# Kernel optimization log

Measured on AMD Instinct MI355X. Metric: run time of the kernel, lower is better.

## Reference

```python
import jax, jax.numpy as jnp
import numpy as np

B, S, NGB, NG, DIM = 64, 4096, 13, 48, 3
NCH = [8, 8, 1]
NSHELLS = 8


def setup_inputs() -> dict:
    key = jax.random.key(0)
    ks = jax.random.split(key, 16)
    rng = np.random.default_rng(0)
    # valid row-wise permutations of the N_ngb neighbor slots per group op
    GnnPerms = jnp.asarray(np.argsort(rng.random((NG, NGB)), axis=1), dtype=jnp.int64)
    NNSites = jax.random.randint(ks[0], (NGB, S), 0, S, dtype=jnp.int64)
    SitesToShells = jax.random.randint(ks[1], (S,), 0, NSHELLS, dtype=jnp.int64)
    # block-diagonal (Ng*dim, Ng*dim) cartesian rotation blocks
    blk = rng.normal(size=(NG, DIM, DIM)).astype(np.float32) * 0.5
    gd = np.zeros((NG * DIM, NG * DIM), np.float32)
    for g in range(NG):
        gd[g * DIM:(g + 1) * DIM, g * DIM:(g + 1) * DIM] = blk[g]
    gdiags = jnp.asarray(gd)
    std = 0.2
    return {
        "InStates": jax.random.normal(ks[2], (B, 1, S), jnp.float32),
        "Psi0": jax.random.normal(ks[3], (NCH[0], 1, NGB), jnp.float32) * std,
        "bias0": jax.random.normal(ks[4], (NCH[0], 1), jnp.float32) * std,
        "Psi1": jax.random.normal(ks[5], (NCH[1], NCH[0], NGB), jnp.float32) * std,
        "bias1": jax.random.normal(ks[6], (NCH[1], 1), jnp.float32) * std,
        "Psi2": jax.random.normal(ks[7], (NCH[2], NCH[1], NGB), jnp.float32) * std,
        "bias2": jax.random.normal(ks[8], (NCH[2], 1), jnp.float32) * std,
        "wtVC": jax.random.normal(ks[9], (DIM, NGB), jnp.float32) * std,
        "ShellWeights": jax.random.normal(ks[10], (NSHELLS,), jnp.float32) * std,
        "gdiags": gdiags,
        "GnnPerms": GnnPerms,
        "NNSites": NNSites,
        "SitesToShells": SitesToShells,
    }


def _rearrange(x, NNSites):
    # x: (B, Nch, S) -> (B, Nch*N_ngb, S); subchannel j of channel c holds x[b, c, NNSites[j, s]]
    b, c, s = x.shape
    return x[:, :, NNSites].reshape(b, c * NGB, s)


def _gconv(x, W, b):
    # x: (B, NchIn*N_ngb, S); W: (NchOut, NchIn, N_ngb); b: (NchOut, 1)
    # group-rotated weights: GW[o, g, c*N_ngb+j] = W[o, c, GnnPerms[g, j]]
    GW = _gconv.GW_cache  # set per-call below via closure-free pattern; replaced in reference
    raise NotImplementedError


def reference(InStates, Psi0, bias0, Psi1, bias1, Psi2, bias2, wtVC,
              ShellWeights, gdiags, GnnPerms, NNSites, SitesToShells):
    act = jax.nn.softplus

    def gconv(x, W, b):
        # rotated weights: (NchOut, Ng, NchIn*N_ngb)
        GW = W[:, :, GnnPerms].transpose(0, 2, 1, 3).reshape(W.shape[0], NG, -1)
        h = jnp.einsum('ogk,bks->bogs', GW, x) + b[:, :, None]  # (B, NchOut, Ng, S)
        return act(h).mean(axis=2)                               # group-orbit average

    out = _rearrange(InStates, NNSites)
    for W, b in ((Psi0, bias0), (Psi1, bias1), (Psi2, bias2)):
        out = gconv(out, W, b)                 # (B, NchOut, S)
        out = _rearrange(out, NNSites)         # (B, NchOut*N_ngb, S)
    # vector channel: row g*dim+d of P is wtVC[d, GnnPerms[g]]
    P = wtVC[:, GnnPerms].transpose(1, 0, 2).reshape(NG * DIM, NGB)
    Wvc = gdiags @ P                           # (Ng*dim, N_ngb)
    v = jnp.einsum('kn,bns->bks', Wvc, out)    # (B, Ng*dim, S)
    v = v.reshape(-1, NG, DIM, out.shape[-1]).mean(axis=1)  # (B, dim, S)
    v = v * ShellWeights[SitesToShells]        # per-site shell weighting
    return v.sum(axis=2) / out.shape[-1]       # (B, dim)
```

## Files before the change

kernel.cpp:

```cpp
#include <hip/hip_runtime.h>
#include <hip/hip_bf16.h>

#define BATCH 64
#define SITES 4096
#define NGB 13
#define NGRP 48
#define SDIM 3

typedef __bf16 bf16x8 __attribute__((ext_vector_type(8)));
typedef float  f32x4  __attribute__((ext_vector_type(4)));

#define OFF_AVC  0
#define OFF_U    64
#define OFF_A0   67648
#define OFF_A1   2164800
#define OFF_PART 4261952
#define UW0H 0
#define UW0L 12288
#define UW1H 24576
#define UW1L 73728
#define UW2H 122880
#define UW2L 129024

__device__ __forceinline__ float softplus_f(float h) {
    return fmaxf(h, 0.f) + __logf(1.f + __expf(-fabsf(h)));
}

__global__ __launch_bounds__(256) void precompute_kernel(
    const float* __restrict__ Psi0, const float* __restrict__ Psi1,
    const float* __restrict__ Psi2, const float* __restrict__ wtVC,
    const float* __restrict__ gdiags, const int* __restrict__ perms,
    float* __restrict__ ws)
{
    float*  Avc = ws + OFF_AVC;
    __bf16* U   = (__bf16*)(ws + OFF_U);
    int t = blockIdx.x * 256 + threadIdx.x;
    if (t < 12288) {
        int k = t & 31, row = t >> 5;
        int o = row / NGRP, g = row - o * NGRP;
        float w = (k < NGB) ? Psi0[o * NGB + perms[g * NGB + k]] : 0.f;
        __bf16 hi = (__bf16)w;
        U[UW0H + t] = hi;
        U[UW0L + t] = (__bf16)(w - (float)hi);
    } else if (t < 61440) {
        int u = t - 12288;
        int k = u & 127, row = u >> 7;
        int o = row / NGRP, g = row - o * NGRP;
        float w = 0.f;
        if (k < 104) { int j = k >> 3, c = k & 7;
                       w = Psi1[(o * 8 + c) * NGB + perms[g * NGB + j]]; }
        __bf16 hi = (__bf16)w;
        U[UW1H + u] = hi;
        U[UW1L + u] = (__bf16)(w - (float)hi);
    } else if (t < 67584) {
        int u = t - 61440;
        int k = u & 127, g = u >> 7;
        float w = 0.f;
        if (k < 104) { int j = k >> 3, c = k & 7;
                       w = Psi2[c * NGB + perms[g * NGB + j]]; }
        __bf16 hi = (__bf16)w;
        U[UW2H + u] = hi;
        U[UW2L + u] = (__bf16)(w - (float)hi);
    } else if (t < 67584 + 39 * NGRP) {
        int t2 = t - 67584;
        int g = t2 % NGRP, u = t2 / NGRP;
        int d = u / NGB, n = u % NGB;
        const int row = g * SDIM + d;
        float s = 0.f;
        for (int k = 0; k < NGRP * SDIM; k++) {
            int g2 = k / SDIM, d2 = k - g2 * SDIM;
            float p = wtVC[d2 * NGB + perms[g2 * NGB + n]];
            s = fmaf(gdiags[row * (NGRP * SDIM) + k], p, s);
        }
        atomicAdd(&Avc[u], s * (1.f / 48.f));
    }
}

template<int NCIN, int NCTOT, int CT, int KPAD, int KSTR, int NWAVES, int NWN,
         int CHUNKS>
__global__ __launch_bounds__(NWAVES * 64) void layer_mfma(
    const float* __restrict__ prev,
    const __bf16* __restrict__ Wh,
    const __bf16* __restrict__ Wl,
    const float* __restrict__ bias,
    const int*   __restrict__ NN,
    float* __restrict__ out)
{
    constexpr int NTHR   = NWAVES * 64;
    constexpr int M      = NCTOT * NGRP;
    constexpr int MTILES = M / 16, NTILES = CT / 16;
    constexpr int NWM    = NWAVES / NWN;
    constexpr int MT_W   = MTILES / NWM, NT_W = NTILES / NWN;
    constexpr int KT     = KPAD / 32;
    constexpr int GS     = NGB * CT;
    constexpr int SPT    = (GS + NTHR - 1) / NTHR;
    constexpr int CPB    = SITES / CT;
    constexpr int BUF    = CT * KSTR;
    constexpr int BPB    = CPB / CHUNKS;

    static_assert(MT_W * 16 == NGRP, "wave covers exactly one o");
    static_assert(NWM * MT_W == MTILES && NWN * NT_W == NTILES, "");
    static_assert((KPAD & 31) == 0 && (KSTR & 7) == 0, "");
    static_assert(CPB % CHUNKS == 0, "block stays within one batch");

    __shared__ __bf16 xh_lds[2 * BUF];
    __shared__ __bf16 xl_lds[2 * BUF];

    const int tid  = threadIdx.x;
    const int wave = tid >> 6, lane = tid & 63;
    const int m16  = lane & 15, quad = lane >> 4;

    const int bid    = blockIdx.x;
    const int b      = bid / BPB;
    const int octet  = bid % BPB;
    const int s0base = octet * (CHUNKS * CT);

    int sj[SPT], scol[SPT];
    bool sv[SPT];
#pragma unroll
    for (int i = 0; i < SPT; i++) {
        int site = tid + i * NTHR;
        sv[i] = (site < GS);
        int ss = sv[i] ? site : 0;
        sj[i] = ss / CT;
        scol[i] = ss % CT;
    }

    auto stage_site = [&](int i, int nn, __bf16* dh, __bf16* dl) {
        if constexpr (NCIN == 1) {
            float v = prev[(size_t)b * SITES + nn];
            __bf16 hi = (__bf16)v;
            dh[scol[i] * KSTR + sj[i]] = hi;
            dl[scol[i] * KSTR + sj[i]] = (__bf16)(v - (float)hi);
        } else {
            const float4* p4 = (const float4*)(prev + ((size_t)(b * SITES + nn)) * 8);
            float4 u0 = p4[0], u1 = p4[1];
            float v[8] = {u0.x, u0.y, u0.z, u0.w, u1.x, u1.y, u1.z, u1.w};
            bf16x8 hv, lv;
#pragma unroll
            for (int c8 = 0; c8 < 8; c8++) {
                __bf16 hi = (__bf16)v[c8];
                hv[c8] = hi;
                lv[c8] = (__bf16)(v[c8] - (float)hi);
            }
            *(bf16x8*)(dh + scol[i] * KSTR + sj[i] * 8) = hv;
            *(bf16x8*)(dl + scol[i] * KSTR + sj[i] * 8) = lv;
        }
    };

    if constexpr (NCIN == 1) {
        for (int e = tid; e < 2 * CT * (KPAD - NGB); e += NTHR) {
            int buf = e / (CT * (KPAD - NGB));
            int r   = e % (CT * (KPAD - NGB));
            int col = r / (KPAD - NGB), p = r % (KPAD - NGB);
            xh_lds[buf * BUF + col * KSTR + NGB + p] = (__bf16)0.f;
            xl_lds[buf * BUF + col * KSTR + NGB + p] = (__bf16)0.f;
        }
    } else {
        const bf16x8 z8 = {};
        for (int e = tid; e < 2 * CT * 3; e += NTHR) {
            int buf = e / (CT * 3);
            int r   = e % (CT * 3);
            int col = r % CT, z = r / CT;
            *(bf16x8*)(xh_lds + buf * BUF + col * KSTR + 104 + z * 8) = z8;
            *(bf16x8*)(xl_lds + buf * BUF + col * KSTR + 104 + z * 8) = z8;
        }
    }

#pragma unroll
    for (int i = 0; i < SPT; i++) if (sv[i]) {
        int nn = NN[sj[i] * SITES + s0base + scol[i]];
        stage_site(i, nn, xh_lds, xl_lds);
    }
    int nnA[SPT];
    if (CHUNKS > 1) {
        const int s1 = s0base + CT;
#pragma unroll
        for (int i = 0; i < SPT; i++)
            nnA[i] = sv[i] ? NN[sj[i] * SITES + s1 + scol[i]] : 0;
    }
    __syncthreads();

    const int wave_mt0 = (wave / NWN) * MT_W;
    const int wave_nt0 = (wave % NWN) * NT_W;
    const int o_g      = (wave_mt0 * 16) / NGRP;
    const float bo     = bias[o_g];

#pragma unroll 1
    for (int c = 0; c < CHUNKS; c++) {
        const int cur = c & 1;
        const __bf16* xh = xh_lds + cur * BUF;
        const __bf16* xl = xl_lds + cur * BUF;

        f32x4 acc[MT_W][NT_W];
#pragma unroll
        for (int mt = 0; mt < MT_W; mt++)
#pragma unroll
            for (int nt = 0; nt < NT_W; nt++) acc[mt][nt] = (f32x4){0.f, 0.f, 0.f, 0.f};

#pragma unroll
        for (int kt = 0; kt < KT; kt++) {
            const int koff = kt * 32 + quad * 8;
            bf16x8 ah[MT_W], al[MT_W], bh[NT_W], bl[NT_W];
#pragma unroll
            for (int mt = 0; mt < MT_W; mt++) {
                int row = (wave_mt0 + mt) * 16 + m16;
                ah[mt] = *(const bf16x8*)(Wh + (size_t)row * KPAD + koff);
                al[mt] = *(const bf16x8*)(Wl + (size_t)row * KPAD + koff);
            }
#pragma unroll
            for (int nt = 0; nt < NT_W; nt++) {
                int cbase = ((wave_nt0 + nt) * 16 + m16) * KSTR + koff;
                bh[nt] = *(const bf16x8*)(xh + cbase);
                bl[nt] = *(const bf16x8*)(xl + cbase);
            }
#pragma unroll
            for (int mt = 0; mt < MT_W; mt++)
#pragma unroll
                for (int nt = 0; nt < NT_W; nt++)
                    acc[mt][nt] = __builtin_amdgcn_mfma_f32_16x16x32_bf16(
                        ah[mt], bh[nt], acc[mt][nt], 0, 0, 0);
#pragma unroll
            for (int mt = 0; mt < MT_W; mt++)
#pragma unroll
                for (int nt = 0; nt < NT_W; nt++)
                    acc[mt][nt] = __builtin_amdgcn_mfma_f32_16x16x32_bf16(
                        al[mt], bh[nt], acc[mt][nt], 0, 0, 0);
#pragma unroll
            for (int mt = 0; mt < MT_W; mt++)
#pragma unroll
                for (int nt = 0; nt < NT_W; nt++)
                    acc[mt][nt] = __builtin_amdgcn_mfma_f32_16x16x32_bf16(
                        ah[mt], bl[nt], acc[mt][nt], 0, 0, 0);
        }

        const int s0c = s0base + c * CT;
#pragma unroll
        for (int nt = 0; nt < NT_W; nt++) {
            float s = 0.f;
#pragma unroll
            for (int mt = 0; mt < MT_W; mt++)
#pragma unroll
                for (int r = 0; r < 4; r++)
                    s += softplus_f(acc[mt][nt][r] + bo);
            s += __shfl_xor(s, 16);
            s += __shfl_xor(s, 32);
            if (quad == 0)
                out[((size_t)(b * SITES + s0c + (wave_nt0 + nt) * 16 + m16)) * NCTOT + o_g]
                    = s * (1.f / 48.f);
        }

        if (c + 1 < CHUNKS) {
            __bf16* dh = xh_lds + (cur ^ 1) * BUF;
            __bf16* dl = xl_lds + (cur ^ 1) * BUF;
#pragma unroll
            for (int i = 0; i < SPT; i++) if (sv[i])
                stage_site(i, nnA[i], dh, dl);
            if (c + 2 < CHUNKS) {
                const int s2 = s0base + (c + 2) * CT;
#pragma unroll
                for (int i = 0; i < SPT; i++)
                    nnA[i] = sv[i] ? NN[sj[i] * SITES + s2 + scol[i]] : 0;
            }
        }
        __syncthreads();
    }
}

__global__ __launch_bounds__(256) void reduce_a(
    const float* __restrict__ A2, const int* __restrict__ NN,
    const int* __restrict__ s2sh, const float* __restrict__ sw,
    const float* __restrict__ Avc, float* __restrict__ partial)
{
    const int b = blockIdx.x >> 4;
    const int chunk = blockIdx.x & 15;
    const int tid = threadIdx.x;
    const int s = (chunk << 8) + tid;
    const float* a = A2 + (size_t)b * SITES;

    float y0 = 0.f, y1 = 0.f, y2 = 0.f;
#pragma unroll
    for (int n = 0; n < NGB; n++) {
        float v = a[NN[n * SITES + s]];
        y0 = fmaf(Avc[n],           v, y0);
        y1 = fmaf(Avc[NGB + n],     v, y1);
        y2 = fmaf(Avc[2 * NGB + n], v, y2);
    }
    const float wgt = sw[s2sh[s]];
    y0 *= wgt; y1 *= wgt; y2 *= wgt;

    __shared__ float red[3][256];
    red[0][tid] = y0; red[1][tid] = y1; red[2][tid] = y2;
    __syncthreads();
    for (int st = 128; st > 0; st >>= 1) {
        if (tid < st) {
            red[0][tid] += red[0][tid + st];
            red[1][tid] += red[1][tid + st];
            red[2][tid] += red[2][tid + st];
        }
        __syncthreads();
    }
    if (tid < 3) partial[(b * 16 + chunk) * 3 + tid] = red[tid][0];
}

__global__ __launch_bounds__(256) void reduce_b(
    const float* __restrict__ partial, float* __restrict__ out)
{
    int t = threadIdx.x;
    if (t < BATCH * 3) {
        int b = t / 3, d = t - b * 3;
        float s = 0.f;
        for (int c = 0; c < 16; c++) s += partial[(b * 16 + c) * 3 + d];
        out[t] = s * (1.f / (float)SITES);
    }
}

extern "C" void kernel_launch(void* const* d_in, const int* in_sizes, int n_in,
                              void* d_out, int out_size, void* d_ws, size_t ws_size,
                              hipStream_t stream)
{
    const float* InStates = (const float*)d_in[0];
    const float* Psi0     = (const float*)d_in[1];
    const float* bias0    = (const float*)d_in[2];
    const float* Psi1     = (const float*)d_in[3];
    const float* bias1    = (const float*)d_in[4];
    const float* Psi2     = (const float*)d_in[5];
    const float* bias2    = (const float*)d_in[6];
    const float* wtVC     = (const float*)d_in[7];
    const float* ShellW   = (const float*)d_in[8];
    const float* gdiags   = (const float*)d_in[9];
    const int*   GnnPerms = (const int*)d_in[10];
    const int*   NNSites  = (const int*)d_in[11];
    const int*   S2Sh     = (const int*)d_in[12];

    float*  ws   = (float*)d_ws;
    float*  Avc  = ws + OFF_AVC;
    __bf16* U    = (__bf16*)(ws + OFF_U);
    float*  A0   = ws + OFF_A0;
    float*  A1   = ws + OFF_A1;
    float*  A2   = ws + OFF_A0;
    float*  PART = ws + OFF_PART;

    float* out = (float*)d_out;

    hipMemsetAsync(Avc, 0, 64 * sizeof(float), stream);
    precompute_kernel<<<272, 256, 0, stream>>>(Psi0, Psi1, Psi2, wtVC, gdiags,
                                               GnnPerms, ws);

    constexpr int CHUNKS = 8;
    constexpr int NBLK   = BATCH * (SITES / 64) / CHUNKS;

    layer_mfma<1, 8, 64, 32, 40, 8, 1, CHUNKS><<<NBLK, 512, 0, stream>>>(
        InStates, U + UW0H, U + UW0L, bias0, NNSites, A0);
    layer_mfma<8, 8, 64, 128, 136, 8, 1, CHUNKS><<<NBLK, 512, 0, stream>>>(
        A0, U + UW1H, U + UW1L, bias1, NNSites, A1);
    layer_mfma<8, 1, 64, 128, 136, 4, 4, CHUNKS><<<NBLK, 256, 0, stream>>>(
        A1, U + UW2H, U + UW2L, bias2, NNSites, A2);

    reduce_a<<<BATCH * 16, 256, 0, stream>>>(A2, NNSites, S2Sh, ShellW, Avc, PART);
    reduce_b<<<1, 256, 0, stream>>>(PART, out);
}
```

Before: 331.5 us.

## Fold final gather-reduce into last layer via transposed site weights and base-2 softplus

Pre-scales all weights and biases by log2(e) so softplus can use the native exp2/log2 instructions, with the 1/48 and ln2 factors folded into one constant. The final neighbour gather and shell-weighted reduction is turned around: a new build_sw kernel scatters, with atomics, per-site weights for the three output dimensions, and the last layer multiplies its outputs by these weights and reduces them in-block. This removes the A2 round trip and the separate reduce_a pass. In exchange it adds a memset, an atomic scatter kernel and a block reduction in LDS, and the atomics make the summation order nondeterministic.

```diff
diff --git a/kernel.cpp b/kernel.cpp
--- a/kernel.cpp
+++ b/kernel.cpp
@@ -7,12 +7,16 @@
 #define NGRP 48
 #define SDIM 3
 
+#define LOG2E 1.44269504f
+#define SPSCALE 0.014440236f
+
 typedef __bf16 bf16x8 __attribute__((ext_vector_type(8)));
 typedef float  f32x4  __attribute__((ext_vector_type(4)));
 
 #define OFF_AVC  0
 #define OFF_U    64
 #define OFF_A0   67648
+#define OFF_SW   67648
 #define OFF_A1   2164800
 #define OFF_PART 4261952
 #define UW0H 0
@@ -22,10 +26,6 @@
 #define UW2H 122880
 #define UW2L 129024
 
-__device__ __forceinline__ float softplus_f(float h) {
-    return fmaxf(h, 0.f) + __logf(1.f + __expf(-fabsf(h)));
-}
-
 __global__ __launch_bounds__(256) void precompute_kernel(
     const float* __restrict__ Psi0, const float* __restrict__ Psi1,
     const float* __restrict__ Psi2, const float* __restrict__ wtVC,
@@ -38,7 +38,7 @@
     if (t < 12288) {
         int k = t & 31, row = t >> 5;
         int o = row / NGRP, g = row - o * NGRP;
-        float w = (k < NGB) ? Psi0[o * NGB + perms[g * NGB + k]] : 0.f;
+        float w = (k < NGB) ? Psi0[o * NGB + perms[g * NGB + k]] * LOG2E : 0.f;
         __bf16 hi = (__bf16)w;
         U[UW0H + t] = hi;
         U[UW0L + t] = (__bf16)(w - (float)hi);
@@ -48,7 +48,7 @@
         int o = row / NGRP, g = row - o * NGRP;
         float w = 0.f;
         if (k < 104) { int j = k >> 3, c = k & 7;
-                       w = Psi1[(o * 8 + c) * NGB + perms[g * NGB + j]]; }
+                       w = Psi1[(o * 8 + c) * NGB + perms[g * NGB + j]] * LOG2E; }
         __bf16 hi = (__bf16)w;
         U[UW1H + u] = hi;
         U[UW1L + u] = (__bf16)(w - (float)hi);
@@ -57,7 +57,7 @@
         int k = u & 127, g = u >> 7;
         float w = 0.f;
         if (k < 104) { int j = k >> 3, c = k & 7;
-                       w = Psi2[c * NGB + perms[g * NGB + j]]; }
+                       w = Psi2[c * NGB + perms[g * NGB + j]] * LOG2E; }
         __bf16 hi = (__bf16)w;
         U[UW2H + u] = hi;
         U[UW2L + u] = (__bf16)(w - (float)hi);
@@ -76,14 +76,32 @@
     }
 }
 
+__global__ __launch_bounds__(256) void build_sw(
+    const float* __restrict__ Avc, const int* __restrict__ NN,
+    const int* __restrict__ s2sh, const float* __restrict__ shellw,
+    float* __restrict__ SW)
+{
+    int e = blockIdx.x * 256 + threadIdx.x;
+    if (e < NGB * SITES) {
+        int n = e / SITES, s = e - n * SITES;
+        float wgt = shellw[s2sh[s]] * (SPSCALE / (float)SITES);
+        int t = NN[e];
+        atomicAdd(&SW[t],             Avc[n] * wgt);
+        atomicAdd(&SW[SITES + t],     Avc[NGB + n] * wgt);
+        atomicAdd(&SW[2 * SITES + t], Avc[2 * NGB + n] * wgt);
+    }
+}
+
 template<int NCIN, int NCTOT, int CT, int KPAD, int KSTR, int NWAVES, int NWN,
-         int CHUNKS>
+         int CHUNKS, int FUSED>
 __global__ __launch_bounds__(NWAVES * 64) void layer_mfma(
     const float* __restrict__ prev,
     const __bf16* __restrict__ Wh,
     const __bf16* __restrict__ Wl,
     const float* __restrict__ bias,
     const int*   __restrict__ NN,
+    const float* __restrict__ SWp,
+    float* __restrict__ partial,
     float* __restrict__ out)
 {
     constexpr int NTHR   = NWAVES * 64;
@@ -167,12 +185,12 @@
         }
     }
 
+    int nnA[SPT];
 #pragma unroll
     for (int i = 0; i < SPT; i++) if (sv[i]) {
         int nn = NN[sj[i] * SITES + s0base + scol[i]];
         stage_site(i, nn, xh_lds, xl_lds);
     }
-    int nnA[SPT];
     if (CHUNKS > 1) {
         const int s1 = s0base + CT;
 #pragma unroll
@@ -184,7 +202,9 @@
     const int wave_mt0 = (wave / NWN) * MT_W;
     const int wave_nt0 = (wave % NWN) * NT_W;
     const int o_g      = (wave_mt0 * 16) / NGRP;
-    const float bo     = bias[o_g];
+    const float bo     = bias[o_g] * LOG2E;
+
+    float y0 = 0.f, y1 = 0.f, y2 = 0.f;
 
 #pragma unroll 1
     for (int c = 0; c < CHUNKS; c++) {
@@ -241,13 +261,22 @@
 #pragma unroll
             for (int mt = 0; mt < MT_W; mt++)
 #pragma unroll
-                for (int r = 0; r < 4; r++)
-                    s += softplus_f(acc[mt][nt][r] + bo);
+                for (int r = 0; r < 4; r++) {
+                    float h = acc[mt][nt][r] + bo;
+                    s += fmaxf(h, 0.f) + __log2f(1.f + exp2f(-fabsf(h)));
+                }
             s += __shfl_xor(s, 16);
             s += __shfl_xor(s, 32);
-            if (quad == 0)
-                out[((size_t)(b * SITES + s0c + (wave_nt0 + nt) * 16 + m16)) * NCTOT + o_g]
-                    = s * (1.f / 48.f);
+            if (quad == 0) {
+                int site = s0c + (wave_nt0 + nt) * 16 + m16;
+                if constexpr (FUSED) {
+                    y0 = fmaf(SWp[site],             s, y0);
+                    y1 = fmaf(SWp[SITES + site],     s, y1);
+                    y2 = fmaf(SWp[2 * SITES + site], s, y2);
+                } else {
+                    out[((size_t)(b * SITES + site)) * NCTOT + o_g] = s * SPSCALE;
+                }
+            }
         }
 
         if (c + 1 < CHUNKS) {
@@ -265,53 +294,34 @@
         }
         __syncthreads();
     }
-}
-
-__global__ __launch_bounds__(256) void reduce_a(
-    const float* __restrict__ A2, const int* __restrict__ NN,
-    const int* __restrict__ s2sh, const float* __restrict__ sw,
-    const float* __restrict__ Avc, float* __restrict__ partial)
-{
-    const int b = blockIdx.x >> 4;
-    const int chunk = blockIdx.x & 15;
-    const int tid = threadIdx.x;
-    const int s = (chunk << 8) + tid;
-    const float* a = A2 + (size_t)b * SITES;
-
-    float y0 = 0.f, y1 = 0.f, y2 = 0.f;
-#pragma unroll
-    for (int n = 0; n < NGB; n++) {
-        float v = a[NN[n * SITES + s]];
-        y0 = fmaf(Avc[n],           v, y0);
-        y1 = fmaf(Avc[NGB + n],     v, y1);
-        y2 = fmaf(Avc[2 * NGB + n], v, y2);
-    }
-    const float wgt = sw[s2sh[s]];
-    y0 *= wgt; y1 *= wgt; y2 *= wgt;
-
-    __shared__ float red[3][256];
-    red[0][tid] = y0; red[1][tid] = y1; red[2][tid] = y2;
-    __syncthreads();
-    for (int st = 128; st > 0; st >>= 1) {
-        if (tid < st) {
-            red[0][tid] += red[0][tid + st];
-            red[1][tid] += red[1][tid + st];
-            red[2][tid] += red[2][tid + st];
-        }
+
+    if constexpr (FUSED) {
+        float* red = (float*)xh_lds;
+        red[tid] = y0;
+        red[NTHR + tid] = y1;
+        red[2 * NTHR + tid] = y2;
         __syncthreads();
-    }
-    if (tid < 3) partial[(b * 16 + chunk) * 3 + tid] = red[tid][0];
-}
-
-__global__ __launch_bounds__(256) void reduce_b(
+        for (int st = NTHR / 2; st > 0; st >>= 1) {
+            if (tid < st) {
+                red[tid] += red[tid + st];
+                red[NTHR + tid] += red[NTHR + tid + st];
+                red[2 * NTHR + tid] += red[2 * NTHR + tid + st];
+            }
+            __syncthreads();
+        }
+        if (tid < 3) partial[bid * 3 + tid] = red[tid * NTHR];
+    }
+}
+
+__global__ __launch_bounds__(256) void final_sum(
     const float* __restrict__ partial, float* __restrict__ out)
 {
     int t = threadIdx.x;
     if (t < BATCH * 3) {
         int b = t / 3, d = t - b * 3;
         float s = 0.f;
-        for (int c = 0; c < 16; c++) s += partial[(b * 16 + c) * 3 + d];
-        out[t] = s * (1.f / (float)SITES);
+        for (int o = 0; o < 8; o++) s += partial[(b * 8 + o) * 3 + d];
+        out[t] = s;
     }
 }
 
@@ -337,8 +347,8 @@
     float*  Avc  = ws + OFF_AVC;
     __bf16* U    = (__bf16*)(ws + OFF_U);
     float*  A0   = ws + OFF_A0;
+    float*  SW   = ws + OFF_SW;
     float*  A1   = ws + OFF_A1;
-    float*  A2   = ws + OFF_A0;
     float*  PART = ws + OFF_PART;
 
     float* out = (float*)d_out;
@@ -350,13 +360,17 @@
     constexpr int CHUNKS = 8;
     constexpr int NBLK   = BATCH * (SITES / 64) / CHUNKS;
 
-    layer_mfma<1, 8, 64, 32, 40, 8, 1, CHUNKS><<<NBLK, 512, 0, stream>>>(
-        InStates, U + UW0H, U + UW0L, bias0, NNSites, A0);
-    layer_mfma<8, 8, 64, 128, 136, 8, 1, CHUNKS><<<NBLK, 512, 0, stream>>>(
-        A0, U + UW1H, U + UW1L, bias1, NNSites, A1);
-    layer_mfma<8, 1, 64, 128, 136, 4, 4, CHUNKS><<<NBLK, 256, 0, stream>>>(
-        A1, U + UW2H, U + UW2L, bias2, NNSites, A2);
-
-    reduce_a<<<BATCH * 16, 256, 0, stream>>>(A2, NNSites, S2Sh, ShellW, Avc, PART);
-    reduce_b<<<1, 256, 0, stream>>>(PART, out);
-}
+    layer_mfma<1, 8, 64, 32, 40, 8, 1, CHUNKS, 0><<<NBLK, 512, 0, stream>>>(
+        InStates, U + UW0H, U + UW0L, bias0, NNSites, nullptr, nullptr, A0);
+    layer_mfma<8, 8, 64, 128, 136, 8, 1, CHUNKS, 0><<<NBLK, 512, 0, stream>>>(
+        A0, U + UW1H, U + UW1L, bias1, NNSites, nullptr, nullptr, A1);
+
+    hipMemsetAsync(SW, 0, 3 * SITES * sizeof(float), stream);
+    build_sw<<<(NGB * SITES + 255) / 256, 256, 0, stream>>>(
+        Avc, NNSites, S2Sh, ShellW, SW);
+
+    layer_mfma<8, 1, 64, 128, 136, 4, 4, CHUNKS, 1><<<NBLK, 256, 0, stream>>>(
+        A1, U + UW2H, U + UW2L, bias2, NNSites, SW, PART, nullptr);
+
+    final_sum<<<1, 256, 0, stream>>>(PART, out);
+}
```

New measurement: 310.6 us. 1.07x faster.
